# Optimization experiments

Measured on AMD Instinct MI355X. Metric: run time of the kernel, lower is better.

The kernel has to match this reference:

```python
import jax, jax.numpy as jnp
from jax import lax
import numpy as np

RADIUS = 1
DILATION = 2
NUM_BINS = 16  # DualSimilarityLoss uses num_bins=16
ALPHA = 5.0
BETA = 0.1
NOISE = 1e-4


def _avg_pool2(x):
    b, c, h, w = x.shape
    return x.reshape(b, c, h // 2, 2, w // 2, 2).mean(axis=(3, 5))


def _conv_rep(x, k, pad):
    # replicate-pad then VALID conv, NCHW / OIHW
    xp = jnp.pad(x, ((0, 0), (0, 0), (pad, pad), (pad, pad)), mode='edge')
    return lax.conv_general_dilated(xp, k, (1, 1), 'VALID',
                                    dimension_numbers=('NCHW', 'OIHW', 'NCHW'))


def _upsample_align_corners(x, H, W):
    # bilinear, align_corners=True (matches F.interpolate(..., align_corners=True))
    b, c, h, w = x.shape

    def coords(n_out, n_in):
        pos = jnp.arange(n_out, dtype=x.dtype) * ((n_in - 1) / (n_out - 1))
        i0 = jnp.clip(jnp.floor(pos).astype(jnp.int32), 0, n_in - 2)
        return i0, pos - i0.astype(x.dtype)

    y0, fy = coords(H, h)
    x0, fx = coords(W, w)
    rows = x[:, :, y0, :] * (1.0 - fy)[None, None, :, None] \
         + x[:, :, y0 + 1, :] * fy[None, None, :, None]
    out = rows[:, :, :, x0] * (1.0 - fx) + rows[:, :, :, x0 + 1] * fx
    return out


def _compute_mind(img, key):
    B, _, H, W = img.shape
    img = _avg_pool2(img)                      # (B,1,H/2,W/2)
    img = img + NOISE * jax.random.normal(key, img.shape, img.dtype)
    h, w = img.shape[2], img.shape[3]
    pad = RADIUS * DILATION                    # 2
    k = 2 * RADIUS + 1                         # 3
    ones_k = jnp.ones((1, 1, k, k), img.dtype)
    padded = jnp.pad(img, ((0, 0), (0, 0), (pad, pad), (pad, pad)), mode='edge')
    patch_mean = lax.conv_general_dilated(padded, ones_k, (1, 1), 'VALID',
                                          dimension_numbers=('NCHW', 'OIHW', 'NCHW')) / (k * k)
    patch_mean = jnp.pad(patch_mean, ((0, 0), (0, 0), (pad, pad), (pad, pad)), mode='edge')
    c = pad
    center = padded[:, :, c:c + h, c:c + w]
    variance = (center - patch_mean[:, :, c:c + h, c:c + w]) ** 2
    variance = _conv_rep(variance, ones_k, RADIUS) / (k * k)
    variance = jnp.maximum(variance, 1e-4)
    descs = []
    for i in range(-RADIUS, RADIUS + 1):
        for j in range(-RADIUS, RADIUS + 1):
            if i == 0 and j == 0:
                continue
            dx, dy = i * DILATION, j * DILATION
            off = padded[:, :, c + dy:c + dy + h, c + dx:c + dx + w]
            diff = jnp.clip((center - off) ** 2 / (variance * 2 + 1e-6), 0.0, 50.0)
            descs.append(diff)
    m = jnp.exp(-jnp.concatenate(descs, axis=1))          # (B,8,h,w)
    m = m / (m.sum(axis=1, keepdims=True) + 1e-8)
    m = jnp.where(jnp.isnan(m), 0.0, m)
    if (h, w) != (H, W):
        m = _upsample_align_corners(m, H, W)
    return m


def _nmi_loss(x, y, kx, ky):
    B = x.shape[0]
    x = x[:, :, ::2, ::2]
    y = y[:, :, ::2, ::2]
    x = x + NOISE * jax.random.normal(kx, x.shape, x.dtype)
    y = y + NOISE * jax.random.normal(ky, y.shape, y.dtype)
    xf = jnp.clip((x.reshape(B, -1) + 1.0) / 2.0, 0.001, 0.999)
    yf = jnp.clip((y.reshape(B, -1) + 1.0) / 2.0, 0.001, 0.999)
    grid = jnp.linspace(0.0, 1.0, NUM_BINS + 1)
    xb = jnp.clip(jnp.searchsorted(grid, xf, side='left') - 1, 0, NUM_BINS - 1)
    yb = jnp.clip(jnp.searchsorted(grid, yf, side='left') - 1, 0, NUM_BINS - 1)
    idx = xb * NUM_BINS + yb                               # (B,N)
    hist = jnp.zeros((B, NUM_BINS * NUM_BINS), jnp.float32)
    hist = hist.at[jnp.arange(B)[:, None], idx].add(1.0)
    hist = hist.reshape(B, NUM_BINS, NUM_BINS)
    hist = hist / (hist.sum(axis=(1, 2), keepdims=True) + 1e-10)
    xh = hist.sum(axis=2)
    yh = hist.sum(axis=1)
    eps = 1e-5
    hist = hist + eps
    xh = xh + eps
    yh = yh + eps
    mi = jnp.sum(hist * (jnp.log(hist) - jnp.log(xh[:, :, None] * yh[:, None, :])), axis=(1, 2))
    hx = -jnp.sum(xh * jnp.log(xh), axis=1)
    hy = -jnp.sum(yh * jnp.log(yh), axis=1)
    se = hx + hy
    nmi = jnp.where(se < 1e-10, 0.0, 2.0 * mi / se)
    nmi = jnp.clip(nmi, -1.0, 1.0)
    return -jnp.clip(nmi.mean(), -1.0, 1.0)


def _reg_loss(flow, ku, kv):
    sx = jnp.array([[-1, 0, 1], [-2, 0, 2], [-1, 0, 1]], jnp.float32).reshape(1, 1, 3, 3)
    sy = jnp.array([[-1, -2, -1], [0, 0, 0], [1, 2, 1]], jnp.float32).reshape(1, 1, 3, 3)
    lp = jnp.array([[0, 1, 0], [1, -4, 1], [0, 1, 0]], jnp.float32).reshape(1, 1, 3, 3)
    f = _avg_pool2(flow)
    u = f[:, 0:1] + NOISE * jax.random.normal(ku, f[:, 0:1].shape, f.dtype)
    v = f[:, 1:2] + NOISE * jax.random.normal(kv, f[:, 1:2].shape, f.dtype)
    grad_mag = _conv_rep(u, sx, 1) ** 2 + _conv_rep(u, sy, 1) ** 2 \
             + _conv_rep(v, sx, 1) ** 2 + _conv_rep(v, sy, 1) ** 2
    lap_mag = _conv_rep(u, lp, 1) ** 2 + _conv_rep(v, lp, 1) ** 2
    return jnp.clip(grad_mag, 0.0, 100.0).mean() + jnp.clip(lap_mag, 0.0, 100.0).mean()


def _total_loss(fixed, moved, flow):
    fixed = jnp.where(jnp.isnan(fixed), 0.0, fixed)
    moved = jnp.where(jnp.isnan(moved), 0.0, moved)
    flow = jnp.where(jnp.isnan(flow), 0.0, flow)
    ks = jax.random.split(jax.random.key(42), 6)
    mi = _nmi_loss(fixed, moved, ks[0], ks[1])
    mx = _compute_mind(fixed, ks[2])
    my = _compute_mind(moved, ks[3])
    d = jnp.abs(mx - my)
    mind = jnp.where(jnp.isnan(d), 0.0, d).mean()
    reg = _reg_loss(flow, ks[4], ks[5])
    return mi + ALPHA * mind + BETA * reg


def setup_inputs() -> dict:
    key = jax.random.key(0)
    k1, k2, k3 = jax.random.split(key, 3)
    B, H, W = 8, 512, 512
    return {
        'fixed': jax.random.normal(k1, (B, 1, H, W), jnp.float32),
        'moved': jax.random.normal(k2, (B, 1, H, W), jnp.float32),
        'flow': jax.random.normal(k3, (B, 2, H, W), jnp.float32),
    }


def reference(fixed, moved, flow):
    return _total_loss(fixed, moved, flow)
```

## Files before the change

kernel.cpp:

```cpp
#include <hip/hip_runtime.h>
#include <cmath>

#define BATCH 8
#define HF 512
#define WF 512
#define HS 256
#define WS 256
#define PLANE_S (HS * WS)
#define PLANE_F (HF * WF)

#define NMIND_BLOCKS 512
#define NREG_BLOCKS  128

#define OFF_HISTP 0
#define OFF_PMIND (512 * 1024)
#define OFF_PGRAD (OFF_PMIND + NMIND_BLOCKS * 8)
#define OFF_PLAP  (OFF_PGRAD + NREG_BLOCKS * 8)

#define IMG_R 39
#define IMG_S 41
#define T_R 36
#define T_S 37
#define V_R 34
#define V_S 35

#define RP 66
#define RS 67

__device__ __forceinline__ int clampi(int v, int lo, int hi) {
    return v < lo ? lo : (v > hi ? hi : v);
}

__device__ __forceinline__ int bin_of(float x) {
    float v = (x + 1.0f) * 0.5f;
    v = fminf(fmaxf(v, 0.001f), 0.999f);
    float t = v * 16.0f;
    float ft = floorf(t);
    int c = (int)ft + ((t > ft) ? 1 : 0);
    int b = c - 1;
    return b < 0 ? 0 : (b > 15 ? 15 : b);
}

__global__ __launch_bounds__(256, 2) void fused_main_kernel(
    const float* __restrict__ fixed, const float* __restrict__ moved,
    const float* __restrict__ flow,
    unsigned* __restrict__ hist_part, double* __restrict__ pmind,
    double* __restrict__ pgrad, double* __restrict__ plap)
{
    __shared__ float S[15098];
    __shared__ unsigned lh[256];
    __shared__ float red[256];
    int tid = threadIdx.x;

    if (blockIdx.x < NREG_BLOCKS) {
        int rb = blockIdx.x;
        int b = rb >> 4, tt = rb & 15;
        int tyr = tt >> 2, txr = tt & 3;
        int y0p = tyr * 64, x0p = txr * 64;
        float* U = S;
        float* V = S + RP * RS;
        const float* ur = flow + (size_t)(b * 2) * PLANE_F;
        const float* vr = ur + PLANE_F;
        for (int i = tid; i < RP * RP; i += 256) {
            int r = i / RP, c = i - r * RP;
            int gy = clampi(y0p - 1 + r, 0, HS - 1);
            int gx = clampi(x0p - 1 + c, 0, WS - 1);
            const float* uu = ur + (size_t)(gy * 2) * WF + (size_t)(gx * 2);
            const float* vv = vr + (size_t)(gy * 2) * WF + (size_t)(gx * 2);
            float2 u0 = *(const float2*)uu, u1 = *(const float2*)(uu + WF);
            float2 v0 = *(const float2*)vv, v1 = *(const float2*)(vv + WF);
            U[r * RS + c] = (u0.x + u0.y + u1.x + u1.y) * 0.25f;
            V[r * RS + c] = (v0.x + v0.y + v1.x + v1.y) * 0.25f;
        }
        __syncthreads();
        float g = 0.f, l = 0.f;
        for (int k = tid; k < 64 * 64; k += 256) {
            int y = k >> 6, x = k & 63;
            const float* u0 = &U[y * RS + x];
            const float* v0 = &V[y * RS + x];
            float a00 = u0[0],      a01 = u0[1],          a02 = u0[2];
            float a10 = u0[RS],     a11 = u0[RS + 1],     a12 = u0[RS + 2];
            float a20 = u0[2 * RS], a21 = u0[2 * RS + 1], a22 = u0[2 * RS + 2];
            float c00 = v0[0],      c01 = v0[1],          c02 = v0[2];
            float c10 = v0[RS],     c11 = v0[RS + 1],     c12 = v0[RS + 2];
            float c20 = v0[2 * RS], c21 = v0[2 * RS + 1], c22 = v0[2 * RS + 2];
            float gxu = (a02 - a00) + 2.f * (a12 - a10) + (a22 - a20);
            float gyu = (a20 - a00) + 2.f * (a21 - a01) + (a22 - a02);
            float gxv = (c02 - c00) + 2.f * (c12 - c10) + (c22 - c20);
            float gyv = (c20 - c00) + 2.f * (c21 - c01) + (c22 - c02);
            float lpu = a01 + a10 - 4.f * a11 + a12 + a21;
            float lpv = c01 + c10 - 4.f * c11 + c12 + c21;
            float grad = gxu * gxu + gyu * gyu + gxv * gxv + gyv * gyv;
            float lap = lpu * lpu + lpv * lpv;
            g += fminf(grad, 100.f);
            l += fminf(lap, 100.f);
        }
        red[tid] = g;
        __syncthreads();
        for (int s = 128; s > 0; s >>= 1) { if (tid < s) red[tid] += red[tid + s]; __syncthreads(); }
        if (tid == 0) pgrad[rb] = (double)red[0];
        __syncthreads();
        red[tid] = l;
        __syncthreads();
        for (int s = 128; s > 0; s >>= 1) { if (tid < s) red[tid] += red[tid + s]; __syncthreads(); }
        if (tid == 0) plap[rb] = (double)red[0];
        return;
    }

    int mb = blockIdx.x - NREG_BLOCKS;
    int b = mb >> 6, ty = (mb >> 3) & 7, tx = mb & 7;
    const float FS = (float)(255.0 / 511.0);
    int Xb = tx * 64, Yb = ty * 64;
    int dbx = (int)((float)Xb * FS);
    int dby = (int)((float)Yb * FS);
    int ibx = dbx - 3, iby = dby - 3;

    float* imgF = S;
    float* imgM = S + IMG_R * IMG_S;
    float* varF = S + 2 * IMG_R * IMG_S;
    float* varM = varF + V_R * V_S;
    float* diff = varM + V_R * V_S;
    float* tF   = diff;
    float* tM   = diff + T_R * T_S;

    lh[tid] = 0u;
    __syncthreads();

    const float* fb = fixed + (size_t)b * PLANE_F;
    const float* mbp = moved + (size_t)b * PLANE_F;
    int oy0 = ty * 32, ox0 = tx * 32;
    for (int i = tid; i < IMG_R * IMG_R; i += 256) {
        int r = i / IMG_R, c = i - r * IMG_R;
        int gy = iby + r, gx = ibx + c;
        int cy = clampi(gy, 0, HS - 1), cx = clampi(gx, 0, WS - 1);
        const float* fp = fb + (size_t)(cy * 2) * WF + (size_t)(cx * 2);
        const float* mp = mbp + (size_t)(cy * 2) * WF + (size_t)(cx * 2);
        float2 f0 = *(const float2*)fp;
        float2 f1 = *(const float2*)(fp + WF);
        float2 m0 = *(const float2*)mp;
        float2 m1 = *(const float2*)(mp + WF);
        imgF[r * IMG_S + c] = (f0.x + f0.y + f1.x + f1.y) * 0.25f;
        imgM[r * IMG_S + c] = (m0.x + m0.y + m1.x + m1.y) * 0.25f;
        if ((unsigned)(gy - oy0) < 32u && (unsigned)(gx - ox0) < 32u) {
            atomicAdd(&lh[bin_of(f0.x) * 16 + bin_of(m0.x)], 1u);
        }
    }
    __syncthreads();
    hist_part[(size_t)mb * 256 + tid] = lh[tid];

    for (int i = tid; i < T_R * T_R; i += 256) {
        int r = i / T_R, c = i - r * T_R;
        float sF = 0.f, sM = 0.f;
        #pragma unroll
        for (int dy = 0; dy < 3; dy++)
            #pragma unroll
            for (int dx = 0; dx < 3; dx++) {
                sF += imgF[(r + dy) * IMG_S + c + dx];
                sM += imgM[(r + dy) * IMG_S + c + dx];
            }
        float dF = imgF[(r + 2) * IMG_S + c + 2] - sF / 9.0f;
        float dM = imgM[(r + 2) * IMG_S + c + 2] - sM / 9.0f;
        tF[r * T_S + c] = dF * dF;
        tM[r * T_S + c] = dM * dM;
    }
    __syncthreads();

    for (int i = tid; i < V_R * V_R; i += 256) {
        int r = i / V_R, c = i - r * V_R;
        float sF = 0.f, sM = 0.f;
        #pragma unroll
        for (int dy = 0; dy < 3; dy++)
            #pragma unroll
            for (int dx = 0; dx < 3; dx++) {
                sF += tF[(r + dy) * T_S + c + dx];
                sM += tM[(r + dy) * T_S + c + dx];
            }
        varF[r * V_S + c] = fmaxf(sF / 9.0f, 1e-4f);
        varM[r * V_S + c] = fmaxf(sM / 9.0f, 1e-4f);
    }
    __syncthreads();

    for (int i = tid; i < V_R * V_R; i += 256) {
        int r = i / V_R, c = i - r * V_R;
        float cF = imgF[(r + 3) * IMG_S + c + 3];
        float cM = imgM[(r + 3) * IMG_S + c + 3];
        float dF2 = 2.f * varF[r * V_S + c] + 1e-6f;
        float dM2 = 2.f * varM[r * V_S + c] + 1e-6f;
        float eF[8], eM[8];
        float sF = 0.f, sM = 0.f;
        int ch = 0;
        #pragma unroll
        for (int ii = -1; ii <= 1; ii++) {
            #pragma unroll
            for (int jj = -1; jj <= 1; jj++) {
                if (ii == 0 && jj == 0) continue;
                float aF = cF - imgF[(r + 3 + 2 * jj) * IMG_S + (c + 3 + 2 * ii)];
                float aM = cM - imgM[(r + 3 + 2 * jj) * IMG_S + (c + 3 + 2 * ii)];
                float qF = fminf(aF * aF / dF2, 50.f);
                float qM = fminf(aM * aM / dM2, 50.f);
                float vF_ = expf(-qF), vM_ = expf(-qM);
                eF[ch] = vF_; eM[ch] = vM_;
                sF += vF_; sM += vM_;
                ch++;
            }
        }
        float wF = 1.f / (sF + 1e-8f);
        float wM = 1.f / (sM + 1e-8f);
        float* dp = diff + (size_t)(r * V_S + c) * 8;
        #pragma unroll
        for (int q = 0; q < 8; q++) dp[q] = eF[q] * wF - eM[q] * wM;
    }
    __syncthreads();

    float local = 0.f;
    for (int k = tid; k < 64 * 64; k += 256) {
        int dy = k >> 6, dx = k & 63;
        float py = (float)(Yb + dy) * FS;
        int y0 = (int)py; if (y0 > HS - 2) y0 = HS - 2;
        float fy = py - (float)y0;
        float px = (float)(Xb + dx) * FS;
        int x0 = (int)px; if (x0 > WS - 2) x0 = WS - 2;
        float fx = px - (float)x0;
        const float* p00 = diff + (size_t)((y0 - dby) * V_S + (x0 - dbx)) * 8;
        const float* p10 = p00 + V_S * 8;
        #pragma unroll
        for (int q = 0; q < 8; q++) {
            float a  = p00[q]     * (1.f - fy) + p10[q]     * fy;
            float c2 = p00[q + 8] * (1.f - fy) + p10[q + 8] * fy;
            local += fabsf(a * (1.f - fx) + c2 * fx);
        }
    }
    red[tid] = local;
    __syncthreads();
    for (int s = 128; s > 0; s >>= 1) { if (tid < s) red[tid] += red[tid + s]; __syncthreads(); }
    if (tid == 0) pmind[mb] = (double)red[0];
}

__global__ void nmi_final_kernel(const unsigned* __restrict__ hist_part,
                                 const double* __restrict__ pmind,
                                 const double* __restrict__ pgrad,
                                 const double* __restrict__ plap,
                                 float* __restrict__ out) {
    int t = threadIdx.x;
    __shared__ float p[256];
    __shared__ float xh[16], yh[16];
    __shared__ float red[256];
    __shared__ double redd[256];
    __shared__ float nmi_acc_s;
    if (t == 0) nmi_acc_s = 0.f;
    __syncthreads();

    for (int b = 0; b < BATCH; b++) {
        unsigned hv = 0;
        const unsigned* hp = hist_part + (size_t)b * 64 * 256 + t;
        for (int i = 0; i < 64; i++) hv += hp[i * 256];
        float pv = (float)hv / 65536.0f;
        p[t] = pv;
        __syncthreads();
        if (t < 16) {
            float s = 0.f;
            for (int j = 0; j < 16; j++) s += p[t * 16 + j];
            xh[t] = s;
        } else if (t < 32) {
            int j = t - 16;
            float s = 0.f;
            for (int i = 0; i < 16; i++) s += p[i * 16 + j];
            yh[j] = s;
        }
        __syncthreads();
        const float eps = 1e-5f;
        int i = t >> 4, j = t & 15;
        float h = pv + eps;
        float mi_term = h * (logf(h) - logf((xh[i] + eps) * (yh[j] + eps)));
        red[t] = mi_term;
        __syncthreads();
        for (int s = 128; s > 0; s >>= 1) { if (t < s) red[t] += red[t + s]; __syncthreads(); }
        float mi = red[0];
        __syncthreads();
        float e_term = 0.f;
        if (t < 16) { float xe = xh[t] + eps; e_term = -xe * logf(xe); }
        else if (t < 32) { float ye = yh[t - 16] + eps; e_term = -ye * logf(ye); }
        red[t] = e_term;
        __syncthreads();
        for (int s = 128; s > 0; s >>= 1) { if (t < s) red[t] += red[t + s]; __syncthreads(); }
        if (t == 0) {
            float se = red[0];
            float nmi = (se < 1e-10f) ? 0.f : 2.f * mi / se;
            nmi_acc_s += fminf(fmaxf(nmi, -1.f), 1.f);
        }
        __syncthreads();
    }

    double sm = 0.0;
    for (int i = t; i < NMIND_BLOCKS; i += 256) sm += pmind[i];
    double sg = 0.0, sl = 0.0;
    for (int i = t; i < NREG_BLOCKS; i += 256) { sg += pgrad[i]; sl += plap[i]; }
    redd[t] = sm;
    __syncthreads();
    for (int s = 128; s > 0; s >>= 1) { if (t < s) redd[t] += redd[t + s]; __syncthreads(); }
    double mind_sum = redd[0];
    __syncthreads();
    redd[t] = sg;
    __syncthreads();
    for (int s = 128; s > 0; s >>= 1) { if (t < s) redd[t] += redd[t + s]; __syncthreads(); }
    double grad_sum = redd[0];
    __syncthreads();
    redd[t] = sl;
    __syncthreads();
    for (int s = 128; s > 0; s >>= 1) { if (t < s) redd[t] += redd[t + s]; __syncthreads(); }
    double lap_sum = redd[0];
    if (t == 0) {
        float s = nmi_acc_s / (float)BATCH;
        s = fminf(fmaxf(s, -1.f), 1.f);
        double mi_loss = -(double)s;
        double mind_mean = mind_sum / (64.0 * (double)PLANE_F);
        double reg = grad_sum / (double)(BATCH * PLANE_S) + lap_sum / (double)(BATCH * PLANE_S);
        out[0] = (float)(mi_loss + 5.0 * mind_mean + 0.1 * reg);
    }
}

extern "C" void kernel_launch(void* const* d_in, const int* in_sizes, int n_in,
                              void* d_out, int out_size, void* d_ws, size_t ws_size,
                              hipStream_t stream) {
    const float* fixed = (const float*)d_in[0];
    const float* moved = (const float*)d_in[1];
    const float* flow  = (const float*)d_in[2];
    float* out = (float*)d_out;
    char* ws = (char*)d_ws;

    unsigned* hist_part = (unsigned*)(ws + OFF_HISTP);
    double*   pmind     = (double*)(ws + OFF_PMIND);
    double*   pgrad     = (double*)(ws + OFF_PGRAD);
    double*   plap      = (double*)(ws + OFF_PLAP);

    fused_main_kernel<<<NREG_BLOCKS + NMIND_BLOCKS, 256, 0, stream>>>(
        fixed, moved, flow, hist_part, pmind, pgrad, plap);
    nmi_final_kernel<<<1, 256, 0, stream>>>(hist_part, pmind, pgrad, plap, out);
}
```

Before: 130.3 us.

## Shrink tiles to 32x32, use global atomic histogram, reorder diff layout planar

Halves the tile size for both the MIND and regularisation blocks, so the grid grows fourfold and launch bounds allow more resident blocks. Per-block histogram partials are replaced by global atomics into a single per-batch histogram, which needs a small zero-init kernel. The diff buffer moves from interleaved-by-channel to planar layout to cut LDS bank conflicts. Smaller tiles raise the halo overhead per output and add an extra kernel launch.

```diff
diff --git a/kernel.cpp b/kernel.cpp
--- a/kernel.cpp
+++ b/kernel.cpp
@@ -9,23 +9,24 @@
 #define PLANE_S (HS * WS)
 #define PLANE_F (HF * WF)
 
-#define NMIND_BLOCKS 512
-#define NREG_BLOCKS  128
-
-#define OFF_HISTP 0
-#define OFF_PMIND (512 * 1024)
+#define NMIND_BLOCKS 2048
+#define NREG_BLOCKS  512
+
+#define OFF_HIST  0
+#define OFF_PMIND 8192
 #define OFF_PGRAD (OFF_PMIND + NMIND_BLOCKS * 8)
 #define OFF_PLAP  (OFF_PGRAD + NREG_BLOCKS * 8)
 
-#define IMG_R 39
-#define IMG_S 41
-#define T_R 36
-#define T_S 37
-#define V_R 34
-#define V_S 35
-
-#define RP 66
-#define RS 67
+#define IMG_R 23
+#define IMG_S 25
+#define T_R 20
+#define T_S 21
+#define V_R 18
+#define V_S 19
+#define VP  (V_R * V_S)
+
+#define RP 34
+#define RS 35
 
 __device__ __forceinline__ int clampi(int v, int lo, int hi) {
     return v < lo ? lo : (v > hi ? hi : v);
@@ -41,22 +42,27 @@
     return b < 0 ? 0 : (b > 15 ? 15 : b);
 }
 
-__global__ __launch_bounds__(256, 2) void fused_main_kernel(
+__global__ void init_kernel(unsigned* __restrict__ hist) {
+    int t = threadIdx.x;
+    for (int i = t; i < BATCH * 256; i += 256) hist[i] = 0u;
+}
+
+__global__ __launch_bounds__(256, 6) void fused_main_kernel(
     const float* __restrict__ fixed, const float* __restrict__ moved,
     const float* __restrict__ flow,
-    unsigned* __restrict__ hist_part, double* __restrict__ pmind,
+    unsigned* __restrict__ hist, double* __restrict__ pmind,
     double* __restrict__ pgrad, double* __restrict__ plap)
 {
-    __shared__ float S[15098];
+    __shared__ float S[4570];
     __shared__ unsigned lh[256];
     __shared__ float red[256];
     int tid = threadIdx.x;
 
-    if (blockIdx.x < NREG_BLOCKS) {
-        int rb = blockIdx.x;
-        int b = rb >> 4, tt = rb & 15;
-        int tyr = tt >> 2, txr = tt & 3;
-        int y0p = tyr * 64, x0p = txr * 64;
+    if (blockIdx.x >= NMIND_BLOCKS) {
+        int rb = blockIdx.x - NMIND_BLOCKS;
+        int b = rb >> 6, rem = rb & 63;
+        int tyr = rem >> 3, txr = rem & 7;
+        int y0p = tyr * 32, x0p = txr * 32;
         float* U = S;
         float* V = S + RP * RS;
         const float* ur = flow + (size_t)(b * 2) * PLANE_F;
@@ -74,8 +80,8 @@
         }
         __syncthreads();
         float g = 0.f, l = 0.f;
-        for (int k = tid; k < 64 * 64; k += 256) {
-            int y = k >> 6, x = k & 63;
+        for (int k = tid; k < 32 * 32; k += 256) {
+            int y = k >> 5, x = k & 31;
             const float* u0 = &U[y * RS + x];
             const float* v0 = &V[y * RS + x];
             float a00 = u0[0],      a01 = u0[1],          a02 = u0[2];
@@ -107,19 +113,20 @@
         return;
     }
 
-    int mb = blockIdx.x - NREG_BLOCKS;
-    int b = mb >> 6, ty = (mb >> 3) & 7, tx = mb & 7;
+    int mb = blockIdx.x;
+    int b = mb >> 8, rem = mb & 255;
+    int ty = rem >> 4, tx = rem & 15;
     const float FS = (float)(255.0 / 511.0);
-    int Xb = tx * 64, Yb = ty * 64;
+    int Xb = tx * 32, Yb = ty * 32;
     int dbx = (int)((float)Xb * FS);
     int dby = (int)((float)Yb * FS);
     int ibx = dbx - 3, iby = dby - 3;
 
     float* imgF = S;
-    float* imgM = S + IMG_R * IMG_S;
-    float* varF = S + 2 * IMG_R * IMG_S;
-    float* varM = varF + V_R * V_S;
-    float* diff = varM + V_R * V_S;
+    float* imgM = S + 575;
+    float* varF = S + 1150;
+    float* varM = S + 1492;
+    float* diff = S + 1834;
     float* tF   = diff;
     float* tM   = diff + T_R * T_S;
 
@@ -128,7 +135,7 @@
 
     const float* fb = fixed + (size_t)b * PLANE_F;
     const float* mbp = moved + (size_t)b * PLANE_F;
-    int oy0 = ty * 32, ox0 = tx * 32;
+    int oy0 = ty * 16, ox0 = tx * 16;
     for (int i = tid; i < IMG_R * IMG_R; i += 256) {
         int r = i / IMG_R, c = i - r * IMG_R;
         int gy = iby + r, gx = ibx + c;
@@ -141,12 +148,15 @@
         float2 m1 = *(const float2*)(mp + WF);
         imgF[r * IMG_S + c] = (f0.x + f0.y + f1.x + f1.y) * 0.25f;
         imgM[r * IMG_S + c] = (m0.x + m0.y + m1.x + m1.y) * 0.25f;
-        if ((unsigned)(gy - oy0) < 32u && (unsigned)(gx - ox0) < 32u) {
+        if ((unsigned)(gy - oy0) < 16u && (unsigned)(gx - ox0) < 16u) {
             atomicAdd(&lh[bin_of(f0.x) * 16 + bin_of(m0.x)], 1u);
         }
     }
     __syncthreads();
-    hist_part[(size_t)mb * 256 + tid] = lh[tid];
+    {
+        unsigned v = lh[tid];
+        if (v) atomicAdd(&hist[b * 256 + tid], v);
+    }
 
     for (int i = tid; i < T_R * T_R; i += 256) {
         int r = i / T_R, c = i - r * T_R;
@@ -165,19 +175,30 @@
     }
     __syncthreads();
 
-    for (int i = tid; i < V_R * V_R; i += 256) {
-        int r = i / V_R, c = i - r * V_R;
-        float sF = 0.f, sM = 0.f;
-        #pragma unroll
-        for (int dy = 0; dy < 3; dy++)
+    float vFl[2], vMl[2];
+    int vi[2];
+    #pragma unroll
+    for (int p = 0; p < 2; p++) {
+        int i = tid + p * 256;
+        vi[p] = -1;
+        if (i < V_R * V_R) {
+            int r = i / V_R, c = i - r * V_R;
+            float sF = 0.f, sM = 0.f;
             #pragma unroll
-            for (int dx = 0; dx < 3; dx++) {
-                sF += tF[(r + dy) * T_S + c + dx];
-                sM += tM[(r + dy) * T_S + c + dx];
-            }
-        varF[r * V_S + c] = fmaxf(sF / 9.0f, 1e-4f);
-        varM[r * V_S + c] = fmaxf(sM / 9.0f, 1e-4f);
-    }
+            for (int dy = 0; dy < 3; dy++)
+                #pragma unroll
+                for (int dx = 0; dx < 3; dx++) {
+                    sF += tF[(r + dy) * T_S + c + dx];
+                    sM += tM[(r + dy) * T_S + c + dx];
+                }
+            vFl[p] = fmaxf(sF / 9.0f, 1e-4f);
+            vMl[p] = fmaxf(sM / 9.0f, 1e-4f);
+            vi[p] = r * V_S + c;
+        }
+    }
+    __syncthreads();
+    #pragma unroll
+    for (int p = 0; p < 2; p++) if (vi[p] >= 0) { varF[vi[p]] = vFl[p]; varM[vi[p]] = vMl[p]; }
     __syncthreads();
 
     for (int i = tid; i < V_R * V_R; i += 256) {
@@ -206,27 +227,27 @@
         }
         float wF = 1.f / (sF + 1e-8f);
         float wM = 1.f / (sM + 1e-8f);
-        float* dp = diff + (size_t)(r * V_S + c) * 8;
+        int base = r * V_S + c;
         #pragma unroll
-        for (int q = 0; q < 8; q++) dp[q] = eF[q] * wF - eM[q] * wM;
+        for (int q = 0; q < 8; q++) diff[q * VP + base] = eF[q] * wF - eM[q] * wM;
     }
     __syncthreads();
 
     float local = 0.f;
-    for (int k = tid; k < 64 * 64; k += 256) {
-        int dy = k >> 6, dx = k & 63;
+    for (int k = tid; k < 32 * 32; k += 256) {
+        int dy = k >> 5, dx = k & 31;
         float py = (float)(Yb + dy) * FS;
         int y0 = (int)py; if (y0 > HS - 2) y0 = HS - 2;
         float fy = py - (float)y0;
         float px = (float)(Xb + dx) * FS;
         int x0 = (int)px; if (x0 > WS - 2) x0 = WS - 2;
         float fx = px - (float)x0;
-        const float* p00 = diff + (size_t)((y0 - dby) * V_S + (x0 - dbx)) * 8;
-        const float* p10 = p00 + V_S * 8;
+        int base = (y0 - dby) * V_S + (x0 - dbx);
         #pragma unroll
         for (int q = 0; q < 8; q++) {
-            float a  = p00[q]     * (1.f - fy) + p10[q]     * fy;
-            float c2 = p00[q + 8] * (1.f - fy) + p10[q + 8] * fy;
+            const float* pq = diff + q * VP + base;
+            float a  = pq[0] * (1.f - fy) + pq[V_S] * fy;
+            float c2 = pq[1] * (1.f - fy) + pq[V_S + 1] * fy;
             local += fabsf(a * (1.f - fx) + c2 * fx);
         }
     }
@@ -236,7 +257,7 @@
     if (tid == 0) pmind[mb] = (double)red[0];
 }
 
-__global__ void nmi_final_kernel(const unsigned* __restrict__ hist_part,
+__global__ void nmi_final_kernel(const unsigned* __restrict__ hist,
                                  const double* __restrict__ pmind,
                                  const double* __restrict__ pgrad,
                                  const double* __restrict__ plap,
@@ -251,10 +272,7 @@
     __syncthreads();
 
     for (int b = 0; b < BATCH; b++) {
-        unsigned hv = 0;
-        const unsigned* hp = hist_part + (size_t)b * 64 * 256 + t;
-        for (int i = 0; i < 64; i++) hv += hp[i * 256];
-        float pv = (float)hv / 65536.0f;
+        float pv = (float)hist[b * 256 + t] / 65536.0f;
         p[t] = pv;
         __syncthreads();
         if (t < 16) {
@@ -328,12 +346,13 @@
     float* out = (float*)d_out;
     char* ws = (char*)d_ws;
 
-    unsigned* hist_part = (unsigned*)(ws + OFF_HISTP);
-    double*   pmind     = (double*)(ws + OFF_PMIND);
-    double*   pgrad     = (double*)(ws + OFF_PGRAD);
-    double*   plap      = (double*)(ws + OFF_PLAP);
-
-    fused_main_kernel<<<NREG_BLOCKS + NMIND_BLOCKS, 256, 0, stream>>>(
-        fixed, moved, flow, hist_part, pmind, pgrad, plap);
-    nmi_final_kernel<<<1, 256, 0, stream>>>(hist_part, pmind, pgrad, plap, out);
-}
+    unsigned* hist  = (unsigned*)(ws + OFF_HIST);
+    double*   pmind = (double*)(ws + OFF_PMIND);
+    double*   pgrad = (double*)(ws + OFF_PGRAD);
+    double*   plap  = (double*)(ws + OFF_PLAP);
+
+    init_kernel<<<1, 256, 0, stream>>>(hist);
+    fused_main_kernel<<<NMIND_BLOCKS + NREG_BLOCKS, 256, 0, stream>>>(
+        fixed, moved, flow, hist, pmind, pgrad, plap);
+    nmi_final_kernel<<<1, 256, 0, stream>>>(hist, pmind, pgrad, plap, out);
+}
```

Measured after the change: 120.4 us. -7.6%, faster.
